# Optimization experiments

Measured on AMD Instinct MI355X. Metric: run time of the kernel, lower is better.

## Reference

```python
import jax, jax.numpy as jnp
import numpy as np

B, S = 8, 2048

def setup_inputs() -> dict:
    key = jax.random.key(0)
    ks = iter(jax.random.split(key, 64))
    def lin(din, dout):
        w = jax.random.normal(next(ks), (din, dout), jnp.float32) / np.float32(np.sqrt(din))
        b = jax.random.normal(next(ks), (dout,), jnp.float32) * 0.01
        return w, b
    inp = {}
    inp['x'] = jax.random.normal(next(ks), (B, S, 256), jnp.float32)
    def blk(tag, d, ff):
        for name, (din, dout) in [('q',(d,d)),('k',(d,d)),('v',(d,d)),('o',(d,d)),('ff1',(d,ff)),('ff2',(ff,d))]:
            w, b = lin(din, dout)
            inp[f'{name}_w{tag}'] = w; inp[f'{name}_b{tag}'] = b
        inp[f'ln1_g{tag}'] = jnp.ones((d,), jnp.float32); inp[f'ln1_b{tag}'] = jnp.zeros((d,), jnp.float32)
        inp[f'ln2_g{tag}'] = jnp.ones((d,), jnp.float32); inp[f'ln2_b{tag}'] = jnp.zeros((d,), jnp.float32)
    blk(1, 256, 1024)
    blk(2, 128, 512)
    for nm, (din, dout) in [('dr1',(256,128)),('dr2',(128,64)),('dr3',(64,32)),('dr4',(32,14))]:
        w, b = lin(din, dout)
        inp[f'{nm}_w'] = w; inp[f'{nm}_b'] = b
    return inp

def _ln(x, g, b, eps=1e-5):
    m = x.mean(-1, keepdims=True)
    v = ((x - m) ** 2).mean(-1, keepdims=True)
    return (x - m) / jnp.sqrt(v + eps) * g + b

def _mha(x, wq, bq, wk, bk, wv, bv, wo, bo, h):
    Bx, Sx, D = x.shape
    hd = D // h
    q = (x @ wq + bq).reshape(Bx, Sx, h, hd).transpose(0, 2, 1, 3)
    k = (x @ wk + bk).reshape(Bx, Sx, h, hd).transpose(0, 2, 1, 3)
    v = (x @ wv + bv).reshape(Bx, Sx, h, hd).transpose(0, 2, 1, 3)
    scores = jnp.einsum('bhqd,bhkd->bhqk', q, k) / jnp.sqrt(jnp.float32(hd))  # [B,h,S,S]
    p = jax.nn.softmax(scores, axis=-1)
    o = jnp.einsum('bhqk,bhkd->bqhd', p, v).reshape(Bx, Sx, D)
    return o @ wo + bo

def _encoder(x, p, h):
    a = _mha(x, p['qw'], p['qb'], p['kw'], p['kb'], p['vw'], p['vb'], p['ow'], p['ob'], h)
    x = _ln(a + x, p['g1'], p['b1'])
    f = jax.nn.relu(x @ p['fw1'] + p['fb1']) @ p['fw2'] + p['fb2']
    return _ln(f + x, p['g2'], p['b2'])

def _pe(s, d):
    pos = jnp.arange(s, dtype=jnp.float32)[:, None]
    dep = jnp.arange(d, dtype=jnp.float32)[None, :]
    ang = pos / jnp.power(jnp.float32(10000.0), dep / d)
    even = (jnp.arange(d)[None, :] % 2) == 0
    return jnp.where(even, jnp.sin(ang), jnp.cos(ang))

def _forward(x,
             q_w1, q_b1, k_w1, k_b1, v_w1, v_b1, o_w1, o_b1,
             ff1_w1, ff1_b1, ff2_w1, ff2_b1, ln1_g1, ln1_b1, ln2_g1, ln2_b1,
             dr1_w, dr1_b,
             q_w2, q_b2, k_w2, k_b2, v_w2, v_b2, o_w2, o_b2,
             ff1_w2, ff1_b2, ff2_w2, ff2_b2, ln1_g2, ln1_b2, ln2_g2, ln2_b2,
             dr2_w, dr2_b, dr3_w, dr3_b, dr4_w, dr4_b):
    h = x + _pe(x.shape[1], x.shape[2])
    p1 = dict(qw=q_w1, qb=q_b1, kw=k_w1, kb=k_b1, vw=v_w1, vb=v_b1, ow=o_w1, ob=o_b1,
              fw1=ff1_w1, fb1=ff1_b1, fw2=ff2_w1, fb2=ff2_b1, g1=ln1_g1, b1=ln1_b1, g2=ln2_g1, b2=ln2_b1)
    h = _encoder(h, p1, 8)
    h = h @ dr1_w + dr1_b
    p2 = dict(qw=q_w2, qb=q_b2, kw=k_w2, kb=k_b2, vw=v_w2, vb=v_b2, ow=o_w2, ob=o_b2,
              fw1=ff1_w2, fb1=ff1_b2, fw2=ff2_w2, fb2=ff2_b2, g1=ln1_g2, b1=ln1_b2, g2=ln2_g2, b2=ln2_b2)
    h = _encoder(h, p2, 8)
    h = h @ dr2_w + dr2_b
    h = jnp.max(h, axis=1)  # AdaptiveMaxPool1d(1) over the sequence dim -> [B, 64]
    h = h @ dr3_w + dr3_b
    return h @ dr4_w + dr4_b  # [B, 14]

def reference(x,
              q_w1, q_b1, k_w1, k_b1, v_w1, v_b1, o_w1, o_b1,
              ff1_w1, ff1_b1, ff2_w1, ff2_b1, ln1_g1, ln1_b1, ln2_g1, ln2_b1,
              dr1_w, dr1_b,
              q_w2, q_b2, k_w2, k_b2, v_w2, v_b2, o_w2, o_b2,
              ff1_w2, ff1_b2, ff2_w2, ff2_b2, ln1_g2, ln1_b2, ln2_g2, ln2_b2,
              dr2_w, dr2_b, dr3_w, dr3_b, dr4_w, dr4_b):
    return _forward(x,
                    q_w1, q_b1, k_w1, k_b1, v_w1, v_b1, o_w1, o_b1,
                    ff1_w1, ff1_b1, ff2_w1, ff2_b1, ln1_g1, ln1_b1, ln2_g1, ln2_b1,
                    dr1_w, dr1_b,
                    q_w2, q_b2, k_w2, k_b2, v_w2, v_b2, o_w2, o_b2,
                    ff1_w2, ff1_b2, ff2_w2, ff2_b2, ln1_g2, ln1_b2, ln2_g2, ln2_b2,
                    dr2_w, dr2_b, dr3_w, dr3_b, dr4_w, dr4_b)
```

## Files before the change

kernel.cpp:

```cpp
#include <hip/hip_runtime.h>
#include <hip/hip_bf16.h>
#include <math.h>

#define SEQ  2048
#define BATCH 8
#define NTOK (SEQ*BATCH)

typedef __attribute__((ext_vector_type(8))) short short8v;
typedef __attribute__((ext_vector_type(4))) float f32x4;
typedef unsigned short u16;

__device__ __forceinline__ u16 f2bf(float f) {
    __hip_bfloat16 h = __float2bfloat16(f);
    return *reinterpret_cast<u16*>(&h);
}
__device__ __forceinline__ float bf2f(u16 u) {
    unsigned v = ((unsigned)u) << 16;
    return *reinterpret_cast<float*>(&v);
}
__device__ __forceinline__ unsigned pack_bf2(float a, float b) {
    __hip_bfloat162 h = __float22bfloat162_rn(float2{a, b});
    return *reinterpret_cast<unsigned*>(&h);
}
__device__ __forceinline__ void gl_lds16(const u16* g, u16* l) {
    __builtin_amdgcn_global_load_lds(
        (const __attribute__((address_space(1))) unsigned int*)g,
        (__attribute__((address_space(3))) unsigned int*)l, 16, 0, 0);
}

struct WDescs {
    const float* src[14];
    int K[14];
    int N[14];
    long dst[14];
    float scale[14];
    int tstart[15];
};

__global__ __launch_bounds__(256) void convert_w_kernel(WDescs d, u16* __restrict__ WA) {
    __shared__ float tile[64][65];
    int blk = blockIdx.x;
    int di = 0;
    while (di < 13 && blk >= d.tstart[di + 1]) ++di;
    int t  = blk - d.tstart[di];
    int K  = d.K[di], N = d.N[di];
    int tn = N >> 6;
    int k0 = (t / tn) << 6, n0 = (t % tn) << 6;
    const float* src = d.src[di];
    float sc = d.scale[di];
    int tid = threadIdx.x;
    #pragma unroll
    for (int i = 0; i < 16; ++i) {
        int id = i * 256 + tid;
        int kk = id >> 6, nn = id & 63;
        tile[kk][nn] = src[(size_t)(k0 + kk) * N + n0 + nn];
    }
    __syncthreads();
    u16* dst = WA + d.dst[di];
    #pragma unroll
    for (int i = 0; i < 16; ++i) {
        int id = i * 256 + tid;
        int nn = id >> 6, kk = id & 63;
        dst[(size_t)(n0 + nn) * K + k0 + kk] = f2bf(tile[kk][nn] * sc);
    }
}

__global__ __launch_bounds__(256) void convert_bias_kernel(
    const float* qb1, const float* kb1, const float* vb1,
    const float* qb2, const float* kb2, const float* vb2,
    const float* dr2b, float* __restrict__ BA, float qs1, float qs2)
{
    int t = blockIdx.x * 256 + threadIdx.x;
    if      (t < 256)  BA[t] = qb1[t] * qs1;
    else if (t < 512)  BA[t] = kb1[t - 256];
    else if (t < 768)  BA[t] = vb1[t - 512];
    else if (t < 896)  BA[t] = qb2[t - 768] * qs2;
    else if (t < 1024) BA[t] = kb2[t - 896];
    else if (t < 1152) BA[t] = vb2[t - 1024];
    else if (t < 1216) BA[t] = dr2b[t - 1152];
    else if (t < 1280) BA[t] = 0.f;
}

__global__ __launch_bounds__(256) void add_pe_kernel(const float* __restrict__ x,
                                                     float* __restrict__ h,
                                                     u16* __restrict__ hb) {
    int idx = blockIdx.x * 256 + threadIdx.x;
    int s = idx >> 8;
    int d = idx & 255;
    float inv = exp2f((float)d * -0.0519051264732f);
    float ang = (float)s * inv;
    float pe  = (d & 1) ? __cosf(ang) : __sinf(ang);
    #pragma unroll
    for (int b = 0; b < BATCH; ++b) {
        size_t g = ((size_t)(b * SEQ + s) << 8) + d;
        float v = x[g] + pe;
        h[g]  = v;
        hb[g] = f2bf(v);
    }
}

template<int BN, int RELU, int WF32, int WBF16, int MAXEP>
__global__ __launch_bounds__(256) void gemm_bf16_kernel(
    const u16* __restrict__ A, const u16* __restrict__ Bt,
    const float* __restrict__ bias, float* __restrict__ Cf,
    u16* __restrict__ Cb, float* __restrict__ Pm, int N, int K)
{
    constexpr int BM  = 64;
    constexpr int NMF = 2;
    constexpr int NBF = BN / 32;
    __shared__ u16 As[2][BM * 64];
    __shared__ u16 Bs[2][BN * 64];
    const int tid  = threadIdx.x;
    const int lane = tid & 63;
    const int c    = lane & 15, g = lane >> 4;
    const int w    = tid >> 6;
    const int wr   = w >> 1, wc = w & 1;
    const size_t bm = (size_t)blockIdx.y * BM;
    const size_t bn = (size_t)blockIdx.x * BN;

    f32x4 acc[NMF][NBF];
    #pragma unroll
    for (int i = 0; i < NMF; ++i)
        #pragma unroll
        for (int j = 0; j < NBF; ++j) acc[i][j] = (f32x4){0.f, 0.f, 0.f, 0.f};

    auto stage = [&](int buf, int t) {
        #pragma unroll
        for (int j = 0; j < BM / 32; ++j) {
            int cid = j * 256 + tid;
            int row = cid >> 3, blk = cid & 7;
            int sof = (blk ^ (row & 7)) * 8;
            gl_lds16(&A[(bm + row) * K + t * 64 + sof], &As[buf][cid * 8]);
        }
        #pragma unroll
        for (int j = 0; j < BN / 32; ++j) {
            int cid = j * 256 + tid;
            int row = cid >> 3, blk = cid & 7;
            int sof = (blk ^ (row & 7)) * 8;
            gl_lds16(&Bt[(bn + row) * K + t * 64 + sof], &Bs[buf][cid * 8]);
        }
    };

    const int nt = K >> 6;
    stage(0, 0);
    __syncthreads();
    for (int t = 0; t < nt; ++t) {
        if (t + 1 < nt) stage((t + 1) & 1, t + 1);
        const int bfi = t & 1;
        #pragma unroll
        for (int ks2 = 0; ks2 < 2; ++ks2) {
            short8v af[NMF], bfr[NBF];
            #pragma unroll
            for (int am = 0; am < NMF; ++am) {
                int r = wr * 32 + am * 16 + c;
                af[am] = *(const short8v*)&As[bfi][r * 64 + (((ks2 * 4 + g) ^ (r & 7)) * 8)];
            }
            #pragma unroll
            for (int bn_ = 0; bn_ < NBF; ++bn_) {
                int r = wc * (BN / 2) + bn_ * 16 + c;
                bfr[bn_] = *(const short8v*)&Bs[bfi][r * 64 + (((ks2 * 4 + g) ^ (r & 7)) * 8)];
            }
            #pragma unroll
            for (int am = 0; am < NMF; ++am)
                #pragma unroll
                for (int bn_ = 0; bn_ < NBF; ++bn_)
                    acc[am][bn_] = __builtin_amdgcn_mfma_f32_16x16x32_bf16(
                                       af[am], bfr[bn_], acc[am][bn_], 0, 0, 0);
        }
        __syncthreads();
    }

    float bv[NBF];
    #pragma unroll
    for (int bn_ = 0; bn_ < NBF; ++bn_) bv[bn_] = bias[bn + wc * (BN / 2) + bn_ * 16 + c];

    if (MAXEP) {
        __shared__ float cm[8][64];
        #pragma unroll
        for (int bn_ = 0; bn_ < NBF; ++bn_) {
            float lm = -INFINITY;
            #pragma unroll
            for (int am = 0; am < NMF; ++am)
                #pragma unroll
                for (int i = 0; i < 4; ++i)
                    lm = fmaxf(lm, acc[am][bn_][i] + bv[bn_]);
            cm[wr * 4 + g][wc * (BN / 2) + bn_ * 16 + c] = lm;
        }
        __syncthreads();
        if (tid < 64) {
            float m = cm[0][tid];
            #pragma unroll
            for (int k = 1; k < 8; ++k) m = fmaxf(m, cm[k][tid]);
            Pm[(size_t)blockIdx.y * 64 + tid] = m;
        }
        return;
    }

    #pragma unroll
    for (int am = 0; am < NMF; ++am) {
        #pragma unroll
        for (int bn_ = 0; bn_ < NBF; ++bn_) {
            #pragma unroll
            for (int i = 0; i < 4; ++i) {
                size_t row = bm + wr * 32 + am * 16 + 4 * g + i;
                size_t col = bn + wc * (BN / 2) + bn_ * 16 + c;
                float v = acc[am][bn_][i] + bv[bn_];
                if (RELU) v = fmaxf(v, 0.f);
                if (WF32)  Cf[row * N + col] = v;
                if (WBF16) Cb[row * N + col] = f2bf(v);
            }
        }
    }
}

template<int D, int WRF>
__global__ __launch_bounds__(256) void ln_residual_kernel(
    const u16* __restrict__ a, const float* __restrict__ r,
    const float* __restrict__ g, const float* __restrict__ bb,
    float* __restrict__ out, u16* __restrict__ outb)
{
    const int N = D >> 6;
    int wave = threadIdx.x >> 6;
    int lane = threadIdx.x & 63;
    size_t token = (size_t)blockIdx.x * 4 + wave;
    const u16*   ar = a + token * D;
    const float* rr = r + token * D;

    float xv[N];
    float s = 0.f;
    #pragma unroll
    for (int i = 0; i < N; ++i) {
        int d = lane + (i << 6);
        xv[i] = bf2f(ar[d]) + rr[d];
        s += xv[i];
    }
    #pragma unroll
    for (int off = 1; off < 64; off <<= 1) s += __shfl_xor(s, off);
    float mean = s * (1.0f / D);
    float vs = 0.f;
    #pragma unroll
    for (int i = 0; i < N; ++i) { float d0 = xv[i] - mean; vs += d0 * d0; }
    #pragma unroll
    for (int off = 1; off < 64; off <<= 1) vs += __shfl_xor(vs, off);
    float inv = 1.0f / sqrtf(vs * (1.0f / D) + 1e-5f);
    #pragma unroll
    for (int i = 0; i < N; ++i) {
        int d = lane + (i << 6);
        float v = (xv[i] - mean) * inv * g[d] + bb[d];
        if (WRF) out[token * D + d] = v;
        outb[token * D + d] = f2bf(v);
    }
}

template<int HD>
__global__ __launch_bounds__(512) void flash_mfma_kernel(
    const u16* __restrict__ QKV, u16* __restrict__ Og, const u16* __restrict__ zsrc)
{
    constexpr int D   = 8 * HD;
    constexpr int SD  = 3 * D;
    constexpr int NDH = HD / 16;

    __shared__ u16 Ks[2][64 * 32];
    __shared__ u16 Vt[2][NDH * 16 * 64];
    __shared__ u16 Pb[128 * 64];

    const int tid  = threadIdx.x;
    const int w    = tid >> 6;
    const int lane = tid & 63;
    const int c    = lane & 15;
    const int g    = lane >> 4;

    const int H    = blockIdx.x + (blockIdx.y << 4);
    const int bh   = H & 63;
    const int qblk = H >> 6;
    const int b = bh >> 3, hh = bh & 7;
    const size_t qvbase = (size_t)b * SEQ * SD + (size_t)hh * HD;
    const size_t obase  = (size_t)b * SEQ * D  + (size_t)hh * HD;
    const int qbase = qblk * 128;

    short8v qf;
    if (HD == 16 && g >= 2) {
        short8v z = {0, 0, 0, 0, 0, 0, 0, 0};
        qf = z;
    } else {
        int qrow = qbase + w * 16 + c;
        qf = *(const short8v*)&QKV[qvbase + (size_t)qrow * SD + 8 * g];
    }

    f32x4 oacc[NDH];
    float lreg[4];
    #pragma unroll
    for (int dh = 0; dh < NDH; ++dh) oacc[dh] = (f32x4){0.f, 0.f, 0.f, 0.f};
    #pragma unroll
    for (int i = 0; i < 4; ++i) lreg[i] = 0.f;

    const bool kstager = (tid < 256);
    const int krow = tid >> 2;
    const int klb  = (tid & 3) ^ ((krow >> 1) & 3);
    const bool kzero = (HD == 16) && (klb >= 2);

    const int vtid = tid - 256;
    const int skey = vtid >> 2;
    const int sch  = (vtid & 3) * 8;
    const bool vstager = (tid >= 256) && (HD == 32 || sch < 16);
    const int spos  = ((skey >> 5) << 5) + 2 * (skey & 15) + ((skey >> 4) & 1);
    const int squad = spos >> 3, soff = spos & 7;
    const int vkc = (c & 7) ^ ((c & 8) >> 1);

    if (kstager)
        gl_lds16(kzero ? zsrc : &QKV[qvbase + (size_t)krow * SD + D + klb * 8],
                 &Ks[0][tid * 8]);
    if (vstager) {
        short8v v0 = *(const short8v*)&QKV[qvbase + (size_t)skey * SD + 2 * D + sch];
        #pragma unroll
        for (int i = 0; i < 8; ++i) {
            int row = sch + i;
            int vk = (row & 7) ^ ((row & 8) >> 1);
            Vt[0][row * 64 + ((squad ^ vk) << 3) + soff] = (u16)v0[i];
        }
    }
    __syncthreads();

    const int NT = SEQ / 64;

    auto tile_body = [&](const int buf, const int t) {
        short8v vv = {0, 0, 0, 0, 0, 0, 0, 0};
        const bool pre = (t + 1 < NT);
        if (pre) {
            if (kstager)
                gl_lds16(kzero ? zsrc
                               : &QKV[qvbase + (size_t)((t + 1) * 64 + krow) * SD + D + klb * 8],
                         &Ks[buf ^ 1][tid * 8]);
            if (vstager)
                vv = *(const short8v*)&QKV[qvbase + (size_t)((t + 1) * 64 + skey) * SD + 2 * D + sch];
        }

        short8v kf[4];
        #pragma unroll
        for (int kh = 0; kh < 4; ++kh) {
            int row = 16 * kh + c;
            kf[kh] = *(const short8v*)&Ks[buf][row * 32 + ((g ^ ((c >> 1) & 3)) * 8)];
        }
        short8v vfr[NDH][2];
        #pragma unroll
        for (int dh = 0; dh < NDH; ++dh) {
            vfr[dh][0] = *(const short8v*)&Vt[buf][(16 * dh + c) * 64 + ((g ^ vkc) << 3)];
            vfr[dh][1] = *(const short8v*)&Vt[buf][(16 * dh + c) * 64 + (((4 + g) ^ vkc) << 3)];
        }

        f32x4 s[4];
        __builtin_amdgcn_s_setprio(1);
        #pragma unroll
        for (int kh = 0; kh < 4; ++kh)
            s[kh] = __builtin_amdgcn_mfma_f32_16x16x32_bf16(
                        qf, kf[kh], (f32x4){0.f, 0.f, 0.f, 0.f}, 0, 0, 0);
        __builtin_amdgcn_s_setprio(0);

        #pragma unroll
        for (int i = 0; i < 4; ++i) {
            float p0 = exp2f(s[0][i]);
            float p1 = exp2f(s[1][i]);
            float p2 = exp2f(s[2][i]);
            float p3 = exp2f(s[3][i]);
            lreg[i] += (p0 + p1) + (p2 + p3);
            int rr = 4 * g + i;
            int pk = (rr & 7) ^ ((rr & 8) >> 1);
            int base = (w * 16 + rr) * 64 + 2 * (c & 3);
            *(unsigned*)&Pb[base + (((c >> 2) ^ pk) << 3)]       = pack_bf2(p0, p1);
            *(unsigned*)&Pb[base + ((((c >> 2) + 4) ^ pk) << 3)] = pack_bf2(p2, p3);
        }

        short8v pf0 = *(const short8v*)&Pb[(w * 16 + c) * 64 + ((g ^ vkc) << 3)];
        short8v pf1 = *(const short8v*)&Pb[(w * 16 + c) * 64 + (((4 + g) ^ vkc) << 3)];
        __builtin_amdgcn_s_setprio(1);
        #pragma unroll
        for (int dh = 0; dh < NDH; ++dh) {
            oacc[dh] = __builtin_amdgcn_mfma_f32_16x16x32_bf16(pf0, vfr[dh][0], oacc[dh], 0, 0, 0);
            oacc[dh] = __builtin_amdgcn_mfma_f32_16x16x32_bf16(pf1, vfr[dh][1], oacc[dh], 0, 0, 0);
        }
        __builtin_amdgcn_s_setprio(0);

        if (pre && vstager) {
            #pragma unroll
            for (int i = 0; i < 8; ++i) {
                int row = sch + i;
                int vk = (row & 7) ^ ((row & 8) >> 1);
                Vt[buf ^ 1][row * 64 + ((squad ^ vk) << 3) + soff] = (u16)vv[i];
            }
        }
        __syncthreads();
    };

    for (int t = 0; t < NT; t += 2) {
        tile_body(0, t);
        tile_body(1, t + 1);
    }

    #pragma unroll
    for (int i = 0; i < 4; ++i) {
        float li = lreg[i];
        li += __shfl_xor(li, 1);
        li += __shfl_xor(li, 2);
        li += __shfl_xor(li, 4);
        li += __shfl_xor(li, 8);
        float inv = 1.0f / li;
        int qrow = qbase + w * 16 + 4 * g + i;
        #pragma unroll
        for (int dh = 0; dh < NDH; ++dh)
            Og[obase + (size_t)qrow * D + 16 * dh + c] = f2bf(oacc[dh][i] * inv);
    }
}

__global__ __launch_bounds__(256) void head_kernel(
    const float* __restrict__ Pm,
    const float* __restrict__ w3, const float* __restrict__ b3,
    const float* __restrict__ w4, const float* __restrict__ b4,
    float* __restrict__ out)
{
    __shared__ float pooled[8][64];
    __shared__ float t2[8][32];
    int tid = threadIdx.x;
    #pragma unroll
    for (int rep = 0; rep < 2; ++rep) {
        int idx = rep * 256 + tid;
        int b = idx >> 6, d = idx & 63;
        float m = -INFINITY;
        #pragma unroll
        for (int k = 0; k < 32; ++k)
            m = fmaxf(m, Pm[(size_t)(b * 32 + k) * 64 + d]);
        pooled[b][d] = m;
    }
    __syncthreads();
    {
        int b = tid >> 5, j = tid & 31;
        float s = b3[j];
        #pragma unroll
        for (int k = 0; k < 64; ++k) s = fmaf(pooled[b][k], w3[k * 32 + j], s);
        t2[b][j] = s;
    }
    __syncthreads();
    if (tid < 8 * 14) {
        int b = tid / 14, j = tid % 14;
        float s = b4[j];
        #pragma unroll
        for (int k = 0; k < 32; ++k) s = fmaf(t2[b][k], w4[k * 14 + j], s);
        out[b * 14 + j] = s;
    }
}

extern "C" void kernel_launch(void* const* d_in, const int* in_sizes, int n_in,
                              void* d_out, int out_size, void* d_ws, size_t ws_size,
                              hipStream_t stream) {
    const float* x     = (const float*)d_in[0];
    const float* qw1   = (const float*)d_in[1];
    const float* qb1   = (const float*)d_in[2];
    const float* kw1   = (const float*)d_in[3];
    const float* kb1   = (const float*)d_in[4];
    const float* vw1   = (const float*)d_in[5];
    const float* vb1   = (const float*)d_in[6];
    const float* ow1   = (const float*)d_in[7];
    const float* ob1   = (const float*)d_in[8];
    const float* f1w1  = (const float*)d_in[9];
    const float* f1b1  = (const float*)d_in[10];
    const float* f2w1  = (const float*)d_in[11];
    const float* f2b1  = (const float*)d_in[12];
    const float* ln1g1 = (const float*)d_in[13];
    const float* ln1b1 = (const float*)d_in[14];
    const float* ln2g1 = (const float*)d_in[15];
    const float* ln2b1 = (const float*)d_in[16];
    const float* qw2   = (const float*)d_in[17];
    const float* qb2   = (const float*)d_in[18];
    const float* kw2   = (const float*)d_in[19];
    const float* kb2   = (const float*)d_in[20];
    const float* vw2   = (const float*)d_in[21];
    const float* vb2   = (const float*)d_in[22];
    const float* ow2   = (const float*)d_in[23];
    const float* ob2   = (const float*)d_in[24];
    const float* f1w2  = (const float*)d_in[25];
    const float* f1b2  = (const float*)d_in[26];
    const float* f2w2  = (const float*)d_in[27];
    const float* f2b2  = (const float*)d_in[28];
    const float* ln1g2 = (const float*)d_in[29];
    const float* ln1b2 = (const float*)d_in[30];
    const float* ln2g2 = (const float*)d_in[31];
    const float* ln2b2 = (const float*)d_in[32];
    const float* dr1w  = (const float*)d_in[33];
    const float* dr1b  = (const float*)d_in[34];
    const float* dr2w  = (const float*)d_in[35];
    const float* dr2b  = (const float*)d_in[36];
    const float* dr3w  = (const float*)d_in[37];
    const float* dr3b  = (const float*)d_in[38];
    const float* dr4w  = (const float*)d_in[39];
    const float* dr4b  = (const float*)d_in[40];

    const size_t T = NTOK;
    float* F1 = (float*)d_ws;
    float* F2 = F1 + T * 256;
    u16*   E1 = (u16*)(F2 + T * 256);
    u16*   E2 = E1 + T * 256;
    u16*   E3 = E2 + T * 256;
    u16*   Dq = E3 + T * 256;
    u16*   WA = Dq + T * 1024;
    float* BA = (float*)(WA + 1048576);
    const u16* ZS = (const u16*)(BA + 1216);

    const float QS1 = 0.25503488f;
    const float QS2 = 0.36067376f;

    WDescs wd;
    const float* srcs[14] = {qw1, kw1, vw1, ow1, f1w1, f2w1, dr1w,
                             qw2, kw2, vw2, ow2, f1w2, f2w2, dr2w};
    int Ks_[14]  = {256, 256, 256, 256, 256, 1024, 256, 128, 128, 128, 128, 128, 512, 128};
    int Ns_[14]  = {256, 256, 256, 256, 1024, 256, 128, 128, 128, 128, 128, 512, 128, 64};
    long dsts[14] = {0, 65536, 131072, 196608, 262144, 524288, 786432,
                     819200, 835584, 851968, 868352, 884736, 950272, 1015808};
    float scs[14] = {QS1, 1.f, 1.f, 1.f, 1.f, 1.f, 1.f, QS2, 1.f, 1.f, 1.f, 1.f, 1.f, 1.f};
    int tst[15] = {0, 16, 32, 48, 64, 128, 192, 200, 204, 208, 212, 216, 232, 248, 250};
    for (int i = 0; i < 14; ++i) {
        wd.src[i] = srcs[i]; wd.K[i] = Ks_[i]; wd.N[i] = Ns_[i];
        wd.dst[i] = dsts[i]; wd.scale[i] = scs[i];
    }
    for (int i = 0; i < 15; ++i) wd.tstart[i] = tst[i];

    const dim3 blk(256);
    const dim3 blk512(512);

    convert_w_kernel<<<250, blk, 0, stream>>>(wd, WA);
    convert_bias_kernel<<<5, blk, 0, stream>>>(qb1, kb1, vb1, qb2, kb2, vb2, dr2b, BA, QS1, QS2);

    add_pe_kernel<<<SEQ, blk, 0, stream>>>(x, F1, E1);

    gemm_bf16_kernel<128,0,0,1,0><<<dim3(6, 256), blk, 0, stream>>>(E1, WA + 0,      BA,   nullptr, Dq, nullptr, 768, 256);
    flash_mfma_kernel<32><<<dim3(16, 64), blk512, 0, stream>>>(Dq, E2, ZS);
    gemm_bf16_kernel< 64,0,0,1,0><<<dim3(4, 256), blk, 0, stream>>>(E2, WA + 196608, ob1,  nullptr, E3, nullptr, 256, 256);
    ln_residual_kernel<256,1><<<NTOK / 4, blk, 0, stream>>>(E3, F1, ln1g1, ln1b1, F1, E1);
    gemm_bf16_kernel<128,1,0,1,0><<<dim3(8, 256), blk, 0, stream>>>(E1, WA + 262144, f1b1, nullptr, Dq, nullptr, 1024, 256);
    gemm_bf16_kernel< 64,0,0,1,0><<<dim3(4, 256), blk, 0, stream>>>(Dq, WA + 524288, f2b1, nullptr, E3, nullptr, 256, 1024);
    ln_residual_kernel<256,1><<<NTOK / 4, blk, 0, stream>>>(E3, F1, ln2g1, ln2b1, F1, E1);

    gemm_bf16_kernel< 64,0,1,1,0><<<dim3(2, 256), blk, 0, stream>>>(E1, WA + 786432, dr1b, F2, E2, nullptr, 128, 256);

    gemm_bf16_kernel<128,0,0,1,0><<<dim3(3, 256), blk, 0, stream>>>(E2, WA + 819200, BA + 768, nullptr, Dq, nullptr, 384, 128);
    flash_mfma_kernel<16><<<dim3(16, 64), blk512, 0, stream>>>(Dq, E3, ZS);
    gemm_bf16_kernel< 64,0,0,1,0><<<dim3(2, 256), blk, 0, stream>>>(E3, WA + 868352, ob2,  nullptr, E2, nullptr, 128, 128);
    ln_residual_kernel<128,1><<<NTOK / 4, blk, 0, stream>>>(E2, F2, ln1g2, ln1b2, F2, E1);
    gemm_bf16_kernel<128,1,0,1,0><<<dim3(4, 256), blk, 0, stream>>>(E1, WA + 884736, f1b2, nullptr, Dq, nullptr, 512, 128);
    gemm_bf16_kernel< 64,0,0,1,0><<<dim3(2, 256), blk, 0, stream>>>(Dq, WA + 950272, f2b2, nullptr, E2, nullptr, 128, 512);
    ln_residual_kernel<128,0><<<NTOK / 4, blk, 0, stream>>>(E2, F2, ln2g2, ln2b2, nullptr, E1);

    gemm_bf16_kernel< 64,0,0,0,1><<<dim3(1, 256), blk, 0, stream>>>(E1, WA + 1015808, BA + 1152, nullptr, nullptr, F1, 64, 128);
    head_kernel<<<1, blk, 0, stream>>>(F1, dr3w, dr3b, dr4w, dr4b, (float*)d_out);
}
```

Measured before the change: 489.9 us.

## Halve flash attention block to 4 waves each handling two query tiles

The flash attention kernel now runs 256 threads (4 waves) instead of 512, and each wave processes two 16-row query tiles, so every K/V fragment loaded from LDS is reused across both tiles. K and V staging is spread over all threads, with V written as packed 32-bit pairs. The P buffer gets a padded row stride of 72, and the setprio hints are removed. Separately, the bias conversion kernel is merged into the weight conversion kernel to save one launch. The change trades fewer waves per block and more registers per thread for less LDS fragment traffic and fewer barriers per unit of work.

```diff
diff --git a/kernel.cpp b/kernel.cpp
--- a/kernel.cpp
+++ b/kernel.cpp
@@ -35,11 +35,29 @@
     long dst[14];
     float scale[14];
     int tstart[15];
+    const float* qb1; const float* kb1; const float* vb1;
+    const float* qb2; const float* kb2; const float* vb2;
+    const float* dr2b;
+    float qs1, qs2;
 };
 
-__global__ __launch_bounds__(256) void convert_w_kernel(WDescs d, u16* __restrict__ WA) {
+__global__ __launch_bounds__(256) void convert_w_kernel(WDescs d, u16* __restrict__ WA,
+                                                        float* __restrict__ BA) {
+    int blk = blockIdx.x;
+    int tid = threadIdx.x;
+    if (blk >= 250) {
+        int t = (blk - 250) * 256 + tid;
+        if      (t < 256)  BA[t] = d.qb1[t] * d.qs1;
+        else if (t < 512)  BA[t] = d.kb1[t - 256];
+        else if (t < 768)  BA[t] = d.vb1[t - 512];
+        else if (t < 896)  BA[t] = d.qb2[t - 768] * d.qs2;
+        else if (t < 1024) BA[t] = d.kb2[t - 896];
+        else if (t < 1152) BA[t] = d.vb2[t - 1024];
+        else if (t < 1216) BA[t] = d.dr2b[t - 1152];
+        else if (t < 1280) BA[t] = 0.f;
+        return;
+    }
     __shared__ float tile[64][65];
-    int blk = blockIdx.x;
     int di = 0;
     while (di < 13 && blk >= d.tstart[di + 1]) ++di;
     int t  = blk - d.tstart[di];
@@ -48,7 +66,6 @@
     int k0 = (t / tn) << 6, n0 = (t % tn) << 6;
     const float* src = d.src[di];
     float sc = d.scale[di];
-    int tid = threadIdx.x;
     #pragma unroll
     for (int i = 0; i < 16; ++i) {
         int id = i * 256 + tid;
@@ -63,22 +80,6 @@
         int nn = id >> 6, kk = id & 63;
         dst[(size_t)(n0 + nn) * K + k0 + kk] = f2bf(tile[kk][nn] * sc);
     }
-}
-
-__global__ __launch_bounds__(256) void convert_bias_kernel(
-    const float* qb1, const float* kb1, const float* vb1,
-    const float* qb2, const float* kb2, const float* vb2,
-    const float* dr2b, float* __restrict__ BA, float qs1, float qs2)
-{
-    int t = blockIdx.x * 256 + threadIdx.x;
-    if      (t < 256)  BA[t] = qb1[t] * qs1;
-    else if (t < 512)  BA[t] = kb1[t - 256];
-    else if (t < 768)  BA[t] = vb1[t - 512];
-    else if (t < 896)  BA[t] = qb2[t - 768] * qs2;
-    else if (t < 1024) BA[t] = kb2[t - 896];
-    else if (t < 1152) BA[t] = vb2[t - 1024];
-    else if (t < 1216) BA[t] = dr2b[t - 1152];
-    else if (t < 1280) BA[t] = 0.f;
 }
 
 __global__ __launch_bounds__(256) void add_pe_kernel(const float* __restrict__ x,
@@ -253,16 +254,17 @@
 }
 
 template<int HD>
-__global__ __launch_bounds__(512) void flash_mfma_kernel(
+__global__ __launch_bounds__(256) void flash_mfma_kernel(
     const u16* __restrict__ QKV, u16* __restrict__ Og, const u16* __restrict__ zsrc)
 {
-    constexpr int D   = 8 * HD;
-    constexpr int SD  = 3 * D;
-    constexpr int NDH = HD / 16;
+    constexpr int D    = 8 * HD;
+    constexpr int SD   = 3 * D;
+    constexpr int NDH  = HD / 16;
+    constexpr int PSTR = 72;
 
     __shared__ u16 Ks[2][64 * 32];
     __shared__ u16 Vt[2][NDH * 16 * 64];
-    __shared__ u16 Pb[128 * 64];
+    __shared__ u16 Pb[128 * PSTR];
 
     const int tid  = threadIdx.x;
     const int w    = tid >> 6;
@@ -278,45 +280,50 @@
     const size_t obase  = (size_t)b * SEQ * D  + (size_t)hh * HD;
     const int qbase = qblk * 128;
 
-    short8v qf;
-    if (HD == 16 && g >= 2) {
-        short8v z = {0, 0, 0, 0, 0, 0, 0, 0};
-        qf = z;
-    } else {
-        int qrow = qbase + w * 16 + c;
-        qf = *(const short8v*)&QKV[qvbase + (size_t)qrow * SD + 8 * g];
-    }
-
-    f32x4 oacc[NDH];
-    float lreg[4];
-    #pragma unroll
-    for (int dh = 0; dh < NDH; ++dh) oacc[dh] = (f32x4){0.f, 0.f, 0.f, 0.f};
-    #pragma unroll
-    for (int i = 0; i < 4; ++i) lreg[i] = 0.f;
-
-    const bool kstager = (tid < 256);
+    short8v qf[2];
+    #pragma unroll
+    for (int qb = 0; qb < 2; ++qb) {
+        if (HD == 16 && g >= 2) {
+            short8v z = {0, 0, 0, 0, 0, 0, 0, 0};
+            qf[qb] = z;
+        } else {
+            int qrow = qbase + w * 32 + qb * 16 + c;
+            qf[qb] = *(const short8v*)&QKV[qvbase + (size_t)qrow * SD + 8 * g];
+        }
+    }
+
+    f32x4 oacc[2][NDH];
+    float lreg[2][4];
+    #pragma unroll
+    for (int qb = 0; qb < 2; ++qb) {
+        #pragma unroll
+        for (int dh = 0; dh < NDH; ++dh) oacc[qb][dh] = (f32x4){0.f, 0.f, 0.f, 0.f};
+        #pragma unroll
+        for (int i = 0; i < 4; ++i) lreg[qb][i] = 0.f;
+    }
+
     const int krow = tid >> 2;
     const int klb  = (tid & 3) ^ ((krow >> 1) & 3);
     const bool kzero = (HD == 16) && (klb >= 2);
-
-    const int vtid = tid - 256;
-    const int skey = vtid >> 2;
-    const int sch  = (vtid & 3) * 8;
-    const bool vstager = (tid >= 256) && (HD == 32 || sch < 16);
-    const int spos  = ((skey >> 5) << 5) + 2 * (skey & 15) + ((skey >> 4) & 1);
-    const int squad = spos >> 3, soff = spos & 7;
+    const int kb    = tid >> 2;
+    const int k0    = (kb & 15) + 32 * (kb >> 4);
+    const int sch   = (tid & 3) * 8;
+    const bool vstager = (tid < 128) && (HD == 32 || sch < 16);
+    const int spos0 = 2 * (k0 & 15) + 32 * (k0 >> 5);
+    const int squad = spos0 >> 3, soff = spos0 & 7;
     const int vkc = (c & 7) ^ ((c & 8) >> 1);
 
-    if (kstager)
-        gl_lds16(kzero ? zsrc : &QKV[qvbase + (size_t)krow * SD + D + klb * 8],
-                 &Ks[0][tid * 8]);
+    gl_lds16(kzero ? zsrc : &QKV[qvbase + (size_t)krow * SD + D + klb * 8],
+             &Ks[0][tid * 8]);
     if (vstager) {
-        short8v v0 = *(const short8v*)&QKV[qvbase + (size_t)skey * SD + 2 * D + sch];
+        short8v va = *(const short8v*)&QKV[qvbase + (size_t)k0 * SD + 2 * D + sch];
+        short8v vb = *(const short8v*)&QKV[qvbase + (size_t)(k0 + 16) * SD + 2 * D + sch];
         #pragma unroll
         for (int i = 0; i < 8; ++i) {
             int row = sch + i;
             int vk = (row & 7) ^ ((row & 8) >> 1);
-            Vt[0][row * 64 + ((squad ^ vk) << 3) + soff] = (u16)v0[i];
+            *(unsigned*)&Vt[0][row * 64 + ((squad ^ vk) << 3) + soff] =
+                ((unsigned)(u16)va[i]) | (((unsigned)(u16)vb[i]) << 16);
         }
     }
     __syncthreads();
@@ -324,15 +331,17 @@
     const int NT = SEQ / 64;
 
     auto tile_body = [&](const int buf, const int t) {
-        short8v vv = {0, 0, 0, 0, 0, 0, 0, 0};
+        short8v vva = {0,0,0,0,0,0,0,0}, vvb = {0,0,0,0,0,0,0,0};
         const bool pre = (t + 1 < NT);
         if (pre) {
-            if (kstager)
-                gl_lds16(kzero ? zsrc
-                               : &QKV[qvbase + (size_t)((t + 1) * 64 + krow) * SD + D + klb * 8],
-                         &Ks[buf ^ 1][tid * 8]);
-            if (vstager)
-                vv = *(const short8v*)&QKV[qvbase + (size_t)((t + 1) * 64 + skey) * SD + 2 * D + sch];
+            gl_lds16(kzero ? zsrc
+                           : &QKV[qvbase + (size_t)((t + 1) * 64 + krow) * SD + D + klb * 8],
+                     &Ks[buf ^ 1][tid * 8]);
+            if (vstager) {
+                const size_t nb = qvbase + (size_t)((t + 1) * 64) * SD + 2 * D + sch;
+                vva = *(const short8v*)&QKV[nb + (size_t)k0 * SD];
+                vvb = *(const short8v*)&QKV[nb + (size_t)(k0 + 16) * SD];
+            }
         }
 
         short8v kf[4];
@@ -348,44 +357,45 @@
             vfr[dh][1] = *(const short8v*)&Vt[buf][(16 * dh + c) * 64 + (((4 + g) ^ vkc) << 3)];
         }
 
-        f32x4 s[4];
-        __builtin_amdgcn_s_setprio(1);
-        #pragma unroll
-        for (int kh = 0; kh < 4; ++kh)
-            s[kh] = __builtin_amdgcn_mfma_f32_16x16x32_bf16(
-                        qf, kf[kh], (f32x4){0.f, 0.f, 0.f, 0.f}, 0, 0, 0);
-        __builtin_amdgcn_s_setprio(0);
-
-        #pragma unroll
-        for (int i = 0; i < 4; ++i) {
-            float p0 = exp2f(s[0][i]);
-            float p1 = exp2f(s[1][i]);
-            float p2 = exp2f(s[2][i]);
-            float p3 = exp2f(s[3][i]);
-            lreg[i] += (p0 + p1) + (p2 + p3);
-            int rr = 4 * g + i;
-            int pk = (rr & 7) ^ ((rr & 8) >> 1);
-            int base = (w * 16 + rr) * 64 + 2 * (c & 3);
-            *(unsigned*)&Pb[base + (((c >> 2) ^ pk) << 3)]       = pack_bf2(p0, p1);
-            *(unsigned*)&Pb[base + ((((c >> 2) + 4) ^ pk) << 3)] = pack_bf2(p2, p3);
-        }
-
-        short8v pf0 = *(const short8v*)&Pb[(w * 16 + c) * 64 + ((g ^ vkc) << 3)];
-        short8v pf1 = *(const short8v*)&Pb[(w * 16 + c) * 64 + (((4 + g) ^ vkc) << 3)];
-        __builtin_amdgcn_s_setprio(1);
-        #pragma unroll
-        for (int dh = 0; dh < NDH; ++dh) {
-            oacc[dh] = __builtin_amdgcn_mfma_f32_16x16x32_bf16(pf0, vfr[dh][0], oacc[dh], 0, 0, 0);
-            oacc[dh] = __builtin_amdgcn_mfma_f32_16x16x32_bf16(pf1, vfr[dh][1], oacc[dh], 0, 0, 0);
-        }
-        __builtin_amdgcn_s_setprio(0);
+        #pragma unroll
+        for (int qb = 0; qb < 2; ++qb) {
+            f32x4 s[4];
+            #pragma unroll
+            for (int kh = 0; kh < 4; ++kh)
+                s[kh] = __builtin_amdgcn_mfma_f32_16x16x32_bf16(
+                            qf[qb], kf[kh], (f32x4){0.f, 0.f, 0.f, 0.f}, 0, 0, 0);
+
+            #pragma unroll
+            for (int i = 0; i < 4; ++i) {
+                float p0 = exp2f(s[0][i]);
+                float p1 = exp2f(s[1][i]);
+                float p2 = exp2f(s[2][i]);
+                float p3 = exp2f(s[3][i]);
+                lreg[qb][i] += (p0 + p1) + (p2 + p3);
+                int rr = 4 * g + i;
+                int pk = (rr & 7) ^ ((rr & 8) >> 1);
+                int base = (w * 32 + qb * 16 + rr) * PSTR + 2 * (c & 3);
+                *(unsigned*)&Pb[base + (((c >> 2) ^ pk) << 3)]       = pack_bf2(p0, p1);
+                *(unsigned*)&Pb[base + ((((c >> 2) + 4) ^ pk) << 3)] = pack_bf2(p2, p3);
+            }
+
+            int prow = (w * 32 + qb * 16 + c) * PSTR;
+            short8v pf0 = *(const short8v*)&Pb[prow + ((g ^ vkc) << 3)];
+            short8v pf1 = *(const short8v*)&Pb[prow + (((4 + g) ^ vkc) << 3)];
+            #pragma unroll
+            for (int dh = 0; dh < NDH; ++dh) {
+                oacc[qb][dh] = __builtin_amdgcn_mfma_f32_16x16x32_bf16(pf0, vfr[dh][0], oacc[qb][dh], 0, 0, 0);
+                oacc[qb][dh] = __builtin_amdgcn_mfma_f32_16x16x32_bf16(pf1, vfr[dh][1], oacc[qb][dh], 0, 0, 0);
+            }
+        }
 
         if (pre && vstager) {
             #pragma unroll
             for (int i = 0; i < 8; ++i) {
                 int row = sch + i;
                 int vk = (row & 7) ^ ((row & 8) >> 1);
-                Vt[buf ^ 1][row * 64 + ((squad ^ vk) << 3) + soff] = (u16)vv[i];
+                *(unsigned*)&Vt[buf ^ 1][row * 64 + ((squad ^ vk) << 3) + soff] =
+                    ((unsigned)(u16)vva[i]) | (((unsigned)(u16)vvb[i]) << 16);
             }
         }
         __syncthreads();
@@ -397,17 +407,20 @@
     }
 
     #pragma unroll
-    for (int i = 0; i < 4; ++i) {
-        float li = lreg[i];
-        li += __shfl_xor(li, 1);
-        li += __shfl_xor(li, 2);
-        li += __shfl_xor(li, 4);
-        li += __shfl_xor(li, 8);
-        float inv = 1.0f / li;
-        int qrow = qbase + w * 16 + 4 * g + i;
-        #pragma unroll
-        for (int dh = 0; dh < NDH; ++dh)
-            Og[obase + (size_t)qrow * D + 16 * dh + c] = f2bf(oacc[dh][i] * inv);
+    for (int qb = 0; qb < 2; ++qb) {
+        #pragma unroll
+        for (int i = 0; i < 4; ++i) {
+            float li = lreg[qb][i];
+            li += __shfl_xor(li, 1);
+            li += __shfl_xor(li, 2);
+            li += __shfl_xor(li, 4);
+            li += __shfl_xor(li, 8);
+            float inv = 1.0f / li;
+            int qrow = qbase + w * 32 + qb * 16 + 4 * g + i;
+            #pragma unroll
+            for (int dh = 0; dh < NDH; ++dh)
+                Og[obase + (size_t)qrow * D + 16 * dh + c] = f2bf(oacc[qb][dh][i] * inv);
+        }
     }
 }
 
@@ -521,17 +534,18 @@
         wd.dst[i] = dsts[i]; wd.scale[i] = scs[i];
     }
     for (int i = 0; i < 15; ++i) wd.tstart[i] = tst[i];
+    wd.qb1 = qb1; wd.kb1 = kb1; wd.vb1 = vb1;
+    wd.qb2 = qb2; wd.kb2 = kb2; wd.vb2 = vb2;
+    wd.dr2b = dr2b; wd.qs1 = QS1; wd.qs2 = QS2;
 
     const dim3 blk(256);
-    const dim3 blk512(512);
-
-    convert_w_kernel<<<250, blk, 0, stream>>>(wd, WA);
-    convert_bias_kernel<<<5, blk, 0, stream>>>(qb1, kb1, vb1, qb2, kb2, vb2, dr2b, BA, QS1, QS2);
+
+    convert_w_kernel<<<256, blk, 0, stream>>>(wd, WA, BA);
 
     add_pe_kernel<<<SEQ, blk, 0, stream>>>(x, F1, E1);
 
     gemm_bf16_kernel<128,0,0,1,0><<<dim3(6, 256), blk, 0, stream>>>(E1, WA + 0,      BA,   nullptr, Dq, nullptr, 768, 256);
-    flash_mfma_kernel<32><<<dim3(16, 64), blk512, 0, stream>>>(Dq, E2, ZS);
+    flash_mfma_kernel<32><<<dim3(16, 64), blk, 0, stream>>>(Dq, E2, ZS);
     gemm_bf16_kernel< 64,0,0,1,0><<<dim3(4, 256), blk, 0, stream>>>(E2, WA + 196608, ob1,  nullptr, E3, nullptr, 256, 256);
     ln_residual_kernel<256,1><<<NTOK / 4, blk, 0, stream>>>(E3, F1, ln1g1, ln1b1, F1, E1);
     gemm_bf16_kernel<128,1,0,1,0><<<dim3(8, 256), blk, 0, stream>>>(E1, WA + 262144, f1b1, nullptr, Dq, nullptr, 1024, 256);
@@ -541,7 +555,7 @@
     gemm_bf16_kernel< 64,0,1,1,0><<<dim3(2, 256), blk, 0, stream>>>(E1, WA + 786432, dr1b, F2, E2, nullptr, 128, 256);
 
     gemm_bf16_kernel<128,0,0,1,0><<<dim3(3, 256), blk, 0, stream>>>(E2, WA + 819200, BA + 768, nullptr, Dq, nullptr, 384, 128);
-    flash_mfma_kernel<16><<<dim3(16, 64), blk512, 0, stream>>>(Dq, E3, ZS);
+    flash_mfma_kernel<16><<<dim3(16, 64), blk, 0, stream>>>(Dq, E3, ZS);
     gemm_bf16_kernel< 64,0,0,1,0><<<dim3(2, 256), blk, 0, stream>>>(E3, WA + 868352, ob2,  nullptr, E2, nullptr, 128, 128);
     ln_residual_kernel<128,1><<<NTOK / 4, blk, 0, stream>>>(E2, F2, ln1g2, ln1b2, F2, E1);
     gemm_bf16_kernel<128,1,0,1,0><<<dim3(4, 256), blk, 0, stream>>>(E1, WA + 884736, f1b2, nullptr, Dq, nullptr, 512, 128);
```

After: 502.7 us. 1.03x slower.
